# Performance work log

Hardware: AMD Instinct MI355X
Metric: run time of the kernel (lower is better)

## Reference

```python
import jax, jax.numpy as jnp
import numpy as np

NUM_HEADS = 16
HEAD_DIM = 64


def _rotate_half(x):
    half = x.shape[-1] // 2
    return jnp.concatenate([-x[..., half:], x[..., :half]], axis=-1)


def setup_inputs() -> dict:
    key = jax.random.key(0)
    ks = jax.random.split(key, 7)
    B, S, C = 4, 2048, 1024
    D = HEAD_DIM
    return {
        "hidden_states": jax.random.normal(ks[0], (B, S, C), dtype=jnp.float32),
        "cos": jax.random.uniform(ks[1], (B, S, D), dtype=jnp.float32),
        "sin": jax.random.uniform(ks[2], (B, S, D), dtype=jnp.float32),
        "qkv_w": jax.random.normal(ks[3], (3 * C, C), dtype=jnp.float32) * (C ** -0.5),
        "qkv_b": jax.random.normal(ks[4], (3 * C,), dtype=jnp.float32) * 0.02,
        "proj_w": jax.random.normal(ks[5], (C, C), dtype=jnp.float32) * (C ** -0.5),
        "proj_b": jax.random.normal(ks[6], (C,), dtype=jnp.float32) * 0.02,
    }


def reference(hidden_states, cos, sin, qkv_w, qkv_b, proj_w, proj_b):
    B, S, C = hidden_states.shape
    H, D = NUM_HEADS, HEAD_DIM
    # Fused QKV projection: [B,S,3C] -> [B,S,3,H,D]
    qkv = (hidden_states @ qkv_w.T + qkv_b).reshape(B, S, 3, H, D)
    q, k, v = qkv[:, :, 0], qkv[:, :, 1], qkv[:, :, 2]  # each [B,S,H,D]
    # 2D RoPE in fp32, cos/sin broadcast over heads
    orig_dtype = q.dtype
    cosf = cos[:, :, None, :].astype(jnp.float32)
    sinf = sin[:, :, None, :].astype(jnp.float32)
    qf = q.astype(jnp.float32)
    kf = k.astype(jnp.float32)
    q = (qf * cosf + _rotate_half(qf) * sinf).astype(orig_dtype)
    k = (kf * cosf + _rotate_half(kf) * sinf).astype(orig_dtype)
    # Scaled dot-product attention (non-causal), default scale 1/sqrt(D)
    scale = D ** -0.5
    scores = jnp.einsum("bqhd,bkhd->bhqk", q, k) * scale  # [B,H,S,S]
    probs = jax.nn.softmax(scores, axis=-1)
    attn = jnp.einsum("bhqk,bkhd->bqhd", probs, v).reshape(B, S, C)
    return attn @ proj_w.T + proj_b
```

## Files before the change

### kernel.cpp

```cpp
#include <hip/hip_runtime.h>
#include <hip/hip_bf16.h>


typedef unsigned short u16;
using bf16x8 = __attribute__((ext_vector_type(8))) __bf16;
using f32x4  = __attribute__((ext_vector_type(4))) float;
using f16x8  = __attribute__((ext_vector_type(8))) _Float16;
using fp16v2 = __attribute__((ext_vector_type(2))) __fp16;

#define LDT 80

__device__ __forceinline__ u16 f2bf(float f) {
  union { float f; unsigned u; } un; un.f = f;
  unsigned r = un.u + 0x7FFFu + ((un.u >> 16) & 1u);
  return (u16)(r >> 16);
}
__device__ __forceinline__ float bf2f(u16 b) {
  union { unsigned u; float f; } un; un.u = ((unsigned)b) << 16;
  return un.f;
}

__device__ __forceinline__ unsigned pkrtz_u32(float a, float b) {
  union { fp16v2 v; unsigned u; } un;
  un.v = __builtin_amdgcn_cvt_pkrtz(a, b);
  return un.u;
}

__device__ __forceinline__ void pswap32(unsigned &x, unsigned &y) {
  asm volatile("v_permlane32_swap_b32 %0, %1" : "+v"(x), "+v"(y));
}
__device__ __forceinline__ void pswap16(unsigned &x, unsigned &y) {
  asm volatile("v_permlane16_swap_b32 %0, %1\n\ts_nop 1" : "+v"(x), "+v"(y));
}

__device__ __forceinline__ void glds16(const void* g, void* l) {
  __builtin_amdgcn_global_load_lds(
      (__attribute__((address_space(1))) void*)(g),
      (__attribute__((address_space(3))) void*)(l), 16, 0, 0);
}

__global__ __launch_bounds__(256) void f2bf_kernel(
    const float* __restrict__ src, u16* __restrict__ dst, int n4)
{
  int i = blockIdx.x * 256 + threadIdx.x;
  if (i < n4) {
    float4 v = ((const float4*)src)[i];
    ushort4 o;
    o.x = f2bf(v.x); o.y = f2bf(v.y); o.z = f2bf(v.z); o.w = f2bf(v.w);
    ((ushort4*)dst)[i] = o;
  }
}

__global__ __launch_bounds__(256) void rope_table_kernel(
    const float* __restrict__ cs, const float* __restrict__ sn,
    u16* __restrict__ RT)
{
  int t = blockIdx.x * 256 + threadIdx.x;
  int lr = t & 15, m = t >> 4;
  const float* c = cs + (size_t)m * 64;
  const float* s = sn + (size_t)m * 64;
  alignas(16) u16 o[8];
  o[0] = f2bf(c[lr]); o[1] = f2bf(c[lr + 16]);
  o[2] = f2bf(c[lr + 32]); o[3] = f2bf(c[lr + 48]);
  o[4] = f2bf(s[lr]); o[5] = f2bf(s[lr + 16]);
  o[6] = f2bf(s[lr + 32]); o[7] = f2bf(s[lr + 48]);
  *(uint4*)(RT + (size_t)t * 8) = *(const uint4*)o;
}

__device__ __forceinline__ void gemm_stage_128(
    const u16* __restrict__ A, const u16* __restrict__ Bm, int K,
    int row0, int col0, int k0, u16* AsB, u16* BsB,
    int w, int lrow, int lcol8)
{
#pragma unroll
  for (int p = 0; p < 4; ++p) {
    int base = w * 32 + p * 8;
    int rr = base + lrow;
    int cc = (lcol8 ^ (rr & 7)) << 3;
    glds16(A  + (size_t)(row0 + rr) * K + k0 + cc, AsB + base * 64);
    glds16(Bm + (size_t)(col0 + rr) * K + k0 + cc, BsB + base * 64);
  }
}

__device__ __forceinline__ void gemm_compute_128(
    const u16* __restrict__ Asc, const u16* __restrict__ Bsc,
    int wm, int wn, int lr, int lq, f32x4 acc[4][4])
{
#pragma unroll
  for (int kx = 0; kx < 2; ++kx) {
    bf16x8 af[4], bv[4];
    const int sl = (((kx << 2) + lq) ^ (lr & 7)) << 3;
#pragma unroll
    for (int i = 0; i < 4; ++i) {
      af[i] = *(const bf16x8*)(&Asc[(wm + i * 16 + lr) * 64 + sl]);
      bv[i] = *(const bf16x8*)(&Bsc[(wn + i * 16 + lr) * 64 + sl]);
    }
#pragma unroll
    for (int i = 0; i < 4; ++i)
#pragma unroll
      for (int j = 0; j < 4; ++j)
        acc[i][j] = __builtin_amdgcn_mfma_f32_16x16x32_bf16(af[i], bv[j], acc[i][j], 0, 0, 0);
  }
}

__device__ __forceinline__ void gemm_core_128(
    const u16* __restrict__ A, const u16* __restrict__ Bm, int K,
    int row0, int col0, u16 (*As)[128 * 64], u16 (*Bs)[128 * 64],
    f32x4 acc[4][4])
{
  const int tid = threadIdx.x;
  const int lane = tid & 63;
  const int w  = tid >> 6;
  const int wm = (w >> 1) << 6;
  const int wn = (w & 1) << 6;
  const int lr = lane & 15;
  const int lq = lane >> 4;
  const int lrow = lane >> 3;
  const int lcol8 = lane & 7;
  const int nk = K >> 6;

  gemm_stage_128(A, Bm, K, row0, col0, 0, As[0], Bs[0], w, lrow, lcol8);

  for (int ks = 0; ks < nk - 1; ++ks) {
    const int cur = ks & 1;
    gemm_stage_128(A, Bm, K, row0, col0, (ks + 1) << 6,
                   As[cur ^ 1], Bs[cur ^ 1], w, lrow, lcol8);
    asm volatile("s_waitcnt vmcnt(8)" ::: "memory");
    __builtin_amdgcn_s_barrier();
    __builtin_amdgcn_sched_barrier(0);
    gemm_compute_128(As[cur], Bs[cur], wm, wn, lr, lq, acc);
    __builtin_amdgcn_sched_barrier(0);
    __builtin_amdgcn_s_barrier();
  }
  asm volatile("s_waitcnt vmcnt(0)" ::: "memory");
  __builtin_amdgcn_s_barrier();
  __builtin_amdgcn_sched_barrier(0);
  gemm_compute_128(As[(nk - 1) & 1], Bs[(nk - 1) & 1], wm, wn, lr, lq, acc);
}

__global__ __launch_bounds__(256) void qkv_gemm_kernel(
    const u16* __restrict__ hs, const u16* __restrict__ wq,
    const float* __restrict__ bias, const u16* __restrict__ RT,
    u16* __restrict__ Q, u16* __restrict__ K, u16* __restrict__ V)
{
  __shared__ __align__(16) u16 As[2][128 * 64];
  __shared__ __align__(16) u16 Bs[2][128 * 64];
  f32x4 acc[4][4];
#pragma unroll
  for (int i = 0; i < 4; ++i)
#pragma unroll
    for (int j = 0; j < 4; ++j) acc[i][j] = (f32x4){0.f, 0.f, 0.f, 0.f};

  const int row0 = blockIdx.y * 128;
  const int col0 = blockIdx.x * 128;
  gemm_core_128(hs, wq, 1024, row0, col0, As, Bs, acc);

  const int lane = threadIdx.x & 63;
  const int w = threadIdx.x >> 6;
  const int lr = lane & 15, lq = lane >> 4;
  const int wm = (w >> 1) << 6, wn = (w & 1) << 6;
  const int ncol = col0 + wn;
  const int wh = ncol >> 10;
  const int h  = (ncol & 1023) >> 6;
  u16* dst = (wh == 0) ? Q : ((wh == 1) ? K : V);
  const float b0 = bias[ncol + lr];
  const float b1 = bias[ncol + 16 + lr];
  const float b2 = bias[ncol + 32 + lr];
  const float b3 = bias[ncol + 48 + lr];

#pragma unroll
  for (int i = 0; i < 4; ++i)
#pragma unroll
    for (int r = 0; r < 4; ++r) {
      int m = row0 + wm + i * 16 + lq * 4 + r;
      float v0 = acc[i][0][r] + b0;
      float v1 = acc[i][1][r] + b1;
      float v2 = acc[i][2][r] + b2;
      float v3 = acc[i][3][r] + b3;
      int b = m >> 11, s = m & 2047;
      size_t off = ((size_t)((b << 4) + h) * 2048 + s) * 64;
      if (wh == 2) {
        union { _Float16 h2; u16 u; } c0, c1, c2, c3;
        c0.h2 = (_Float16)v0; c1.h2 = (_Float16)v1;
        c2.h2 = (_Float16)v2; c3.h2 = (_Float16)v3;
        dst[off + lr]      = c0.u;
        dst[off + 16 + lr] = c1.u;
        dst[off + 32 + lr] = c2.u;
        dst[off + 48 + lr] = c3.u;
      } else {
        alignas(16) u16 rv[8];
        *(uint4*)rv = *(const uint4*)(RT + ((size_t)m * 16 + lr) * 8);
        float o0 = v0 * bf2f(rv[0]) - v2 * bf2f(rv[4]);
        float o1 = v1 * bf2f(rv[1]) - v3 * bf2f(rv[5]);
        float o2 = v2 * bf2f(rv[2]) + v0 * bf2f(rv[6]);
        float o3 = v3 * bf2f(rv[3]) + v1 * bf2f(rv[7]);
        float sc8 = (wh == 0) ? 0.1803368801f : 1.0f;
        dst[off + lr]      = f2bf(o0 * sc8);
        dst[off + 16 + lr] = f2bf(o1 * sc8);
        dst[off + 32 + lr] = f2bf(o2 * sc8);
        dst[off + 48 + lr] = f2bf(o3 * sc8);
      }
    }
}

__global__ __launch_bounds__(256) void vtrans_kernel(
    const u16* __restrict__ V, u16* __restrict__ Vt)
{
  __shared__ __align__(16) u16 T[64][LDT];
  const int bh = blockIdx.y;
  const int s0 = blockIdx.x * 64;
  const u16* src = V + ((size_t)bh * 2048 + s0) * 64;
  const int r = threadIdx.x >> 2;
  const int c = (threadIdx.x & 3) << 4;
  *(uint4*)(&T[r][c])     = *(const uint4*)(src + r * 64 + c);
  *(uint4*)(&T[r][c + 8]) = *(const uint4*)(src + r * 64 + c + 8);
  __syncthreads();
  alignas(16) u16 tmp[16];
#pragma unroll
  for (int j = 0; j < 16; ++j) tmp[j] = T[c + j][r];
  u16* dst = Vt + ((size_t)bh * 64 + r) * 2048 + s0 + c;
  *(uint4*)(dst)     = *(uint4*)(&tmp[0]);
  *(uint4*)(dst + 8) = *(uint4*)(&tmp[8]);
}

__device__ __forceinline__ void attn_stage(
    const u16* __restrict__ Kh, const u16* __restrict__ Vh, int kv0,
    u16* KsB, u16* VsB, int w, int lrow, int lcol8)
{
#pragma unroll
  for (int p = 0; p < 2; ++p) {
    int base = w * 16 + p * 8;
    int rr = base + lrow;
    int cc = (lcol8 ^ (rr & 7)) << 3;
    glds16(Kh + (size_t)(kv0 + rr) * 64 + cc, KsB + base * 64);
    glds16(Vh + (size_t)rr * 2048 + kv0 + cc, VsB + base * 64);
  }
}

__global__ __launch_bounds__(256, 4) void attn_kernel(
    const u16* __restrict__ Q, const u16* __restrict__ K,
    const u16* __restrict__ Vt, u16* __restrict__ O)
{
  __shared__ __align__(16) u16 Ks[2][64 * 64];
  __shared__ __align__(16) u16 Vs[2][64 * 64];
  const int flat = blockIdx.x + (blockIdx.y << 4);
  const int xcd = flat & 7, j = flat >> 3;
  const int bh = (xcd << 3) + (j & 7);
  const int q0 = (j >> 3) << 7;
  const int b = bh >> 4, h = bh & 15;
  const u16* Qh = Q  + (size_t)bh * (2048 * 64);
  const u16* Kh = K  + (size_t)bh * (2048 * 64);
  const u16* Vh = Vt + (size_t)bh * (64 * 2048);
  const int tid = threadIdx.x, lane = tid & 63, w = tid >> 6;
  const int lr = lane & 15, lq = lane >> 4;
  const int lrow = lane >> 3, lcol8 = lane & 7;
  const int wq0 = w * 32;

  attn_stage(Kh, Vh, 0, Ks[0], Vs[0], w, lrow, lcol8);

  bf16x8 qa[2][2];
#pragma unroll
  for (int mi = 0; mi < 2; ++mi)
#pragma unroll
    for (int kx = 0; kx < 2; ++kx)
      qa[mi][kx] = *(const bf16x8*)(Qh + (size_t)(q0 + wq0 + mi * 16 + lr) * 64 + kx * 32 + lq * 8);

  const f32x4 Z = (f32x4){0.f, 0.f, 0.f, 0.f};
  const f16x8 ones = {(_Float16)1.f, (_Float16)1.f, (_Float16)1.f, (_Float16)1.f,
                      (_Float16)1.f, (_Float16)1.f, (_Float16)1.f, (_Float16)1.f};

  f32x4 acc_o[2][4];
  f32x4 ssum[2];
#pragma unroll
  for (int mi = 0; mi < 2; ++mi) {
    ssum[mi] = (f32x4){0.f, 0.f, 0.f, 0.f};
#pragma unroll
    for (int td = 0; td < 4; ++td) acc_o[mi][td] = (f32x4){0.f, 0.f, 0.f, 0.f};
  }

  for (int it = 0; it < 32; ++it) {
    const int cur = it & 1;
    __syncthreads();
    if (it + 1 < 32)
      attn_stage(Kh, Vh, (it + 1) << 6, Ks[cur ^ 1], Vs[cur ^ 1], w, lrow, lcol8);
    const u16* Kc = Ks[cur];
    const u16* Vc = Vs[cur];

    f32x4 st[4][2];
#pragma unroll
    for (int kx = 0; kx < 2; ++kx) {
      bf16x8 ka[4];
#pragma unroll
      for (int tj = 0; tj < 4; ++tj) {
        int row = tj * 16 + lr;
        ka[tj] = *(const bf16x8*)(&Kc[row * 64 + ((((kx << 2) + lq) ^ (lr & 7)) << 3)]);
      }
#pragma unroll
      for (int tj = 0; tj < 4; ++tj)
#pragma unroll
        for (int mi = 0; mi < 2; ++mi)
          st[tj][mi] = __builtin_amdgcn_mfma_f32_16x16x32_bf16(
              ka[tj], qa[mi][kx], kx ? st[tj][mi] : Z, 0, 0, 0);
    }

    f16x8 pa[2][2];
#pragma unroll
    for (int mi = 0; mi < 2; ++mi)
#pragma unroll
      for (int t32 = 0; t32 < 2; ++t32) {
        unsigned dw[4];
#pragma unroll
        for (int tt = 0; tt < 2; ++tt) {
          const int tj = t32 * 2 + tt;
          float e0 = __builtin_amdgcn_exp2f(st[tj][mi][0]);
          float e1 = __builtin_amdgcn_exp2f(st[tj][mi][1]);
          float e2 = __builtin_amdgcn_exp2f(st[tj][mi][2]);
          float e3 = __builtin_amdgcn_exp2f(st[tj][mi][3]);
          dw[tt * 2 + 0] = pkrtz_u32(e0, e1);
          dw[tt * 2 + 1] = pkrtz_u32(e2, e3);
        }
        pswap32(dw[0], dw[2]);
        pswap32(dw[1], dw[3]);
        pswap16(dw[0], dw[2]);
        pswap16(dw[1], dw[3]);
        union { unsigned u[4]; f16x8 v; } P;
        P.u[0] = dw[0]; P.u[1] = dw[1]; P.u[2] = dw[2]; P.u[3] = dw[3];
        pa[mi][t32] = P.v;
      }

#pragma unroll
    for (int t32 = 0; t32 < 2; ++t32) {
      f16x8 bv[4];
#pragma unroll
      for (int td = 0; td < 4; ++td) {
        int row = td * 16 + lr;
        bv[td] = *(const f16x8*)(&Vc[row * 64 + ((((t32 << 2) + lq) ^ (lr & 7)) << 3)]);
      }
#pragma unroll
      for (int td = 0; td < 4; ++td)
#pragma unroll
        for (int mi = 0; mi < 2; ++mi)
          acc_o[mi][td] = __builtin_amdgcn_mfma_f32_16x16x32_f16(pa[mi][t32], bv[td], acc_o[mi][td], 0, 0, 0);
#pragma unroll
      for (int mi = 0; mi < 2; ++mi)
        ssum[mi] = __builtin_amdgcn_mfma_f32_16x16x32_f16(pa[mi][t32], ones, ssum[mi], 0, 0, 0);
    }
  }

#pragma unroll
  for (int mi = 0; mi < 2; ++mi)
#pragma unroll
    for (int r = 0; r < 4; ++r) {
      float inv = 1.f / ssum[mi][r];
      int qq = q0 + wq0 + mi * 16 + lq * 4 + r;
#pragma unroll
      for (int td = 0; td < 4; ++td) {
        int d = td * 16 + lr;
        O[(size_t)(b * 2048 + qq) * 1024 + h * 64 + d] = f2bf(acc_o[mi][td][r] * inv);
      }
    }
}

__global__ __launch_bounds__(256) void proj_gemm_kernel(
    const u16* __restrict__ X, const u16* __restrict__ wp,
    const float* __restrict__ bias, float* __restrict__ out)
{
  __shared__ __align__(16) u16 As[2][128 * 64];
  __shared__ __align__(16) u16 Bs[2][128 * 64];
  f32x4 acc[4][4];
#pragma unroll
  for (int i = 0; i < 4; ++i)
#pragma unroll
    for (int j = 0; j < 4; ++j) acc[i][j] = (f32x4){0.f, 0.f, 0.f, 0.f};

  const int row0 = blockIdx.y * 128;
  const int col0 = blockIdx.x * 128;
  gemm_core_128(X, wp, 1024, row0, col0, As, Bs, acc);

  const int lane = threadIdx.x & 63;
  const int w = threadIdx.x >> 6;
  const int wm = (w >> 1) << 6, wn = (w & 1) << 6;
#pragma unroll
  for (int i = 0; i < 4; ++i)
#pragma unroll
    for (int j = 0; j < 4; ++j)
#pragma unroll
      for (int r = 0; r < 4; ++r) {
        int m = row0 + wm + i * 16 + ((lane >> 4) << 2) + r;
        int n = col0 + wn + j * 16 + (lane & 15);
        out[(size_t)m * 1024 + n] = acc[i][j][r] + bias[n];
      }
}

extern "C" void kernel_launch(void* const* d_in, const int* in_sizes, int n_in,
                              void* d_out, int out_size, void* d_ws, size_t ws_size,
                              hipStream_t stream)
{
  const float* hs   = (const float*)d_in[0];
  const float* cs   = (const float*)d_in[1];
  const float* sn   = (const float*)d_in[2];
  const float* qkvw = (const float*)d_in[3];
  const float* qkvb = (const float*)d_in[4];
  const float* pw   = (const float*)d_in[5];
  const float* pb   = (const float*)d_in[6];
  float* out = (float*)d_out;

  const size_t NQ = (size_t)8192 * 1024;
  u16* hsb   = (u16*)d_ws;
  u16* qkvwb = hsb + NQ;
  u16* pwb   = qkvwb + 3145728;
  u16* Qb    = pwb + 1048576;
  u16* Kb    = Qb + NQ;
  u16* Vb    = Kb + NQ;
  u16* Vtb   = Vb + NQ;
  u16* RT    = Vtb + NQ;
  u16* Ob    = hsb;

  f2bf_kernel<<<8192, 256, 0, stream>>>(hs, hsb, (int)(NQ / 4));
  f2bf_kernel<<<3072, 256, 0, stream>>>(qkvw, qkvwb, 3145728 / 4);
  f2bf_kernel<<<1024, 256, 0, stream>>>(pw, pwb, 1048576 / 4);
  rope_table_kernel<<<512, 256, 0, stream>>>(cs, sn, RT);

  qkv_gemm_kernel<<<dim3(24, 64), 256, 0, stream>>>(hsb, qkvwb, qkvb, RT, Qb, Kb, Vb);
  vtrans_kernel<<<dim3(32, 64), 256, 0, stream>>>(Vb, Vtb);
  attn_kernel<<<dim3(16, 64), 256, 0, stream>>>(Qb, Kb, Vtb, Ob);
  proj_gemm_kernel<<<dim3(8, 64), 256, 0, stream>>>(Ob, pwb, pb, out);
}
```

Baseline: 293.8 us.

## Enlarge QKV and projection GEMM tiles to 256x128 with 512-thread blocks

Both GEMM kernels move from 128x128 tiles with 4 waves to 256x128 tiles with 8 waves. Each block now reuses its B tile across twice as many rows, and the grid height is halved. The main loop is restructured so A for the next step is prefetched before compute. B for the next step is issued between the two k-halves of the MFMA work, and s_setprio is raised around the MFMA bursts. LDS use per block rises to 96KB, which limits residency to one block per CU and may leave fewer blocks to balance across CUs.

```diff
diff --git a/kernel.cpp b/kernel.cpp
--- a/kernel.cpp
+++ b/kernel.cpp
@@ -67,9 +67,9 @@
   *(uint4*)(RT + (size_t)t * 8) = *(const uint4*)o;
 }
 
-__device__ __forceinline__ void gemm_stage_128(
-    const u16* __restrict__ A, const u16* __restrict__ Bm, int K,
-    int row0, int col0, int k0, u16* AsB, u16* BsB,
+
+__device__ __forceinline__ void g2_stageA(
+    const u16* __restrict__ A, int K, int row0, int k0, u16* AsB,
     int w, int lrow, int lcol8)
 {
 #pragma unroll
@@ -77,35 +77,45 @@
     int base = w * 32 + p * 8;
     int rr = base + lrow;
     int cc = (lcol8 ^ (rr & 7)) << 3;
-    glds16(A  + (size_t)(row0 + rr) * K + k0 + cc, AsB + base * 64);
+    glds16(A + (size_t)(row0 + rr) * K + k0 + cc, AsB + base * 64);
+  }
+}
+__device__ __forceinline__ void g2_stageB(
+    const u16* __restrict__ Bm, int K, int col0, int k0, u16* BsB,
+    int w, int lrow, int lcol8)
+{
+#pragma unroll
+  for (int p = 0; p < 2; ++p) {
+    int base = w * 16 + p * 8;
+    int rr = base + lrow;
+    int cc = (lcol8 ^ (rr & 7)) << 3;
     glds16(Bm + (size_t)(col0 + rr) * K + k0 + cc, BsB + base * 64);
   }
 }
 
-__device__ __forceinline__ void gemm_compute_128(
-    const u16* __restrict__ Asc, const u16* __restrict__ Bsc,
+__device__ __forceinline__ void g2_compute_kx(
+    const u16* __restrict__ Asc, const u16* __restrict__ Bsc, int kx,
     int wm, int wn, int lr, int lq, f32x4 acc[4][4])
 {
-#pragma unroll
-  for (int kx = 0; kx < 2; ++kx) {
-    bf16x8 af[4], bv[4];
-    const int sl = (((kx << 2) + lq) ^ (lr & 7)) << 3;
-#pragma unroll
-    for (int i = 0; i < 4; ++i) {
-      af[i] = *(const bf16x8*)(&Asc[(wm + i * 16 + lr) * 64 + sl]);
-      bv[i] = *(const bf16x8*)(&Bsc[(wn + i * 16 + lr) * 64 + sl]);
-    }
-#pragma unroll
-    for (int i = 0; i < 4; ++i)
-#pragma unroll
-      for (int j = 0; j < 4; ++j)
-        acc[i][j] = __builtin_amdgcn_mfma_f32_16x16x32_bf16(af[i], bv[j], acc[i][j], 0, 0, 0);
-  }
-}
-
-__device__ __forceinline__ void gemm_core_128(
+  bf16x8 af[4], bv[4];
+  const int sl = (((kx << 2) + lq) ^ (lr & 7)) << 3;
+#pragma unroll
+  for (int i = 0; i < 4; ++i) {
+    af[i] = *(const bf16x8*)(&Asc[(wm + i * 16 + lr) * 64 + sl]);
+    bv[i] = *(const bf16x8*)(&Bsc[(wn + i * 16 + lr) * 64 + sl]);
+  }
+  __builtin_amdgcn_s_setprio(1);
+#pragma unroll
+  for (int i = 0; i < 4; ++i)
+#pragma unroll
+    for (int j = 0; j < 4; ++j)
+      acc[i][j] = __builtin_amdgcn_mfma_f32_16x16x32_bf16(af[i], bv[j], acc[i][j], 0, 0, 0);
+  __builtin_amdgcn_s_setprio(0);
+}
+
+__device__ __forceinline__ void gemm_core_256x128(
     const u16* __restrict__ A, const u16* __restrict__ Bm, int K,
-    int row0, int col0, u16 (*As)[128 * 64], u16 (*Bs)[128 * 64],
+    int row0, int col0, u16 (*As)[256 * 64], u16 (*Bs)[128 * 64],
     f32x4 acc[4][4])
 {
   const int tid = threadIdx.x;
@@ -119,31 +129,34 @@
   const int lcol8 = lane & 7;
   const int nk = K >> 6;
 
-  gemm_stage_128(A, Bm, K, row0, col0, 0, As[0], Bs[0], w, lrow, lcol8);
-
-  for (int ks = 0; ks < nk - 1; ++ks) {
+  g2_stageA(A, K, row0, 0, As[0], w, lrow, lcol8);
+  g2_stageB(Bm, K, col0, 0, Bs[0], w, lrow, lcol8);
+
+  for (int ks = 0; ks < nk; ++ks) {
     const int cur = ks & 1;
-    gemm_stage_128(A, Bm, K, row0, col0, (ks + 1) << 6,
-                   As[cur ^ 1], Bs[cur ^ 1], w, lrow, lcol8);
-    asm volatile("s_waitcnt vmcnt(8)" ::: "memory");
+    if (ks + 1 < nk) {
+      g2_stageA(A, K, row0, (ks + 1) << 6, As[cur ^ 1], w, lrow, lcol8);
+      asm volatile("s_waitcnt vmcnt(4)" ::: "memory");
+    } else {
+      asm volatile("s_waitcnt vmcnt(0)" ::: "memory");
+    }
     __builtin_amdgcn_s_barrier();
     __builtin_amdgcn_sched_barrier(0);
-    gemm_compute_128(As[cur], Bs[cur], wm, wn, lr, lq, acc);
+    g2_compute_kx(As[cur], Bs[cur], 0, wm, wn, lr, lq, acc);
+    if (ks + 1 < nk)
+      g2_stageB(Bm, K, col0, (ks + 1) << 6, Bs[cur ^ 1], w, lrow, lcol8);
+    g2_compute_kx(As[cur], Bs[cur], 1, wm, wn, lr, lq, acc);
     __builtin_amdgcn_sched_barrier(0);
     __builtin_amdgcn_s_barrier();
   }
-  asm volatile("s_waitcnt vmcnt(0)" ::: "memory");
-  __builtin_amdgcn_s_barrier();
-  __builtin_amdgcn_sched_barrier(0);
-  gemm_compute_128(As[(nk - 1) & 1], Bs[(nk - 1) & 1], wm, wn, lr, lq, acc);
-}
-
-__global__ __launch_bounds__(256) void qkv_gemm_kernel(
+}
+
+__global__ __launch_bounds__(512, 2) void qkv_gemm_kernel(
     const u16* __restrict__ hs, const u16* __restrict__ wq,
     const float* __restrict__ bias, const u16* __restrict__ RT,
     u16* __restrict__ Q, u16* __restrict__ K, u16* __restrict__ V)
 {
-  __shared__ __align__(16) u16 As[2][128 * 64];
+  __shared__ __align__(16) u16 As[2][256 * 64];
   __shared__ __align__(16) u16 Bs[2][128 * 64];
   f32x4 acc[4][4];
 #pragma unroll
@@ -151,9 +164,9 @@
 #pragma unroll
     for (int j = 0; j < 4; ++j) acc[i][j] = (f32x4){0.f, 0.f, 0.f, 0.f};
 
-  const int row0 = blockIdx.y * 128;
+  const int row0 = blockIdx.y * 256;
   const int col0 = blockIdx.x * 128;
-  gemm_core_128(hs, wq, 1024, row0, col0, As, Bs, acc);
+  gemm_core_256x128(hs, wq, 1024, row0, col0, As, Bs, acc);
 
   const int lane = threadIdx.x & 63;
   const int w = threadIdx.x >> 6;
@@ -361,11 +374,11 @@
     }
 }
 
-__global__ __launch_bounds__(256) void proj_gemm_kernel(
+__global__ __launch_bounds__(512, 2) void proj_gemm_kernel(
     const u16* __restrict__ X, const u16* __restrict__ wp,
     const float* __restrict__ bias, float* __restrict__ out)
 {
-  __shared__ __align__(16) u16 As[2][128 * 64];
+  __shared__ __align__(16) u16 As[2][256 * 64];
   __shared__ __align__(16) u16 Bs[2][128 * 64];
   f32x4 acc[4][4];
 #pragma unroll
@@ -373,9 +386,9 @@
 #pragma unroll
     for (int j = 0; j < 4; ++j) acc[i][j] = (f32x4){0.f, 0.f, 0.f, 0.f};
 
-  const int row0 = blockIdx.y * 128;
+  const int row0 = blockIdx.y * 256;
   const int col0 = blockIdx.x * 128;
-  gemm_core_128(X, wp, 1024, row0, col0, As, Bs, acc);
+  gemm_core_256x128(X, wp, 1024, row0, col0, As, Bs, acc);
 
   const int lane = threadIdx.x & 63;
   const int w = threadIdx.x >> 6;
@@ -421,8 +434,8 @@
   f2bf_kernel<<<1024, 256, 0, stream>>>(pw, pwb, 1048576 / 4);
   rope_table_kernel<<<512, 256, 0, stream>>>(cs, sn, RT);
 
-  qkv_gemm_kernel<<<dim3(24, 64), 256, 0, stream>>>(hsb, qkvwb, qkvb, RT, Qb, Kb, Vb);
+  qkv_gemm_kernel<<<dim3(24, 32), 512, 0, stream>>>(hsb, qkvwb, qkvb, RT, Qb, Kb, Vb);
   vtrans_kernel<<<dim3(32, 64), 256, 0, stream>>>(Vb, Vtb);
   attn_kernel<<<dim3(16, 64), 256, 0, stream>>>(Qb, Kb, Vtb, Ob);
-  proj_gemm_kernel<<<dim3(8, 64), 256, 0, stream>>>(Ob, pwb, pb, out);
-}
+  proj_gemm_kernel<<<dim3(8, 32), 512, 0, stream>>>(Ob, pwb, pb, out);
+}
```

Result: slower. 305.5 us (+4.0%).
